# Kernel tuning notes

Measured on AMD Instinct MI355X. Metric: run time of the kernel, lower is better.

The kernel has to match this reference:

```python
import jax
jax.config.update("jax_enable_x64", True)
import jax.numpy as jnp
import numpy as np

# Paillier parameters (small primes so all modular arithmetic is exact in int64)
P, Q = 59, 61
N = P * Q                    # 3599, public modulus
N2 = N * N                   # 12,952,801; (N2-1)^2 < 2^63 -> int64-safe
LAM = (P - 1) * (Q - 1) // np.gcd(P - 1, Q - 1)   # lcm(p-1, q-1) = 870
MU = pow(int(LAM), -1, int(N))                     # lambda^{-1} mod n (g = n+1 variant)
LAM_BITS = [(LAM >> i) & 1 for i in range(int(LAM).bit_length())]  # LSB-first, static


def _decrypt(c):
    """Batched Paillier decryption: m = L(c^lambda mod n^2) * mu mod n, L(x)=(x-1)//n."""
    b = c % N2
    r = jnp.ones_like(b)
    # static square-and-multiply over the 10 bits of lambda (fully unrolled, elementwise)
    for bit in LAM_BITS:
        if bit:
            r = (r * b) % N2
        b = (b * b) % N2
    return ((r - 1) // N * MU) % N


def setup_inputs() -> dict:
    key = jax.random.key(0)
    k1, _ = jax.random.split(key)
    c = jax.random.randint(k1, (8192, 4096), 1, N2, dtype=jnp.int64)
    inv_scale = jnp.ones((1,), dtype=jnp.float32)
    return {"c": c, "inv_scale": inv_scale}


def reference(c, inv_scale):
    dec = _decrypt(c).astype(jnp.float32)
    # original: activation(decrypt(c) / 1000); inv_scale == 1.0 keeps math identical
    return jax.nn.relu(dec * (inv_scale / 1000.0))
```

## Files before the change

### kernel.cpp

```cpp
#include <hip/hip_runtime.h>
#include <stdint.h>

static constexpr uint32_t PP  = 59, QQ = 61;
static constexpr uint32_t Nn  = PP * QQ;
static constexpr uint32_t P2  = PP * PP;
static constexpr uint32_t Q2  = QQ * QQ;
static constexpr uint32_t LAM = 1740;

constexpr uint32_t cinv(uint32_t a, uint32_t m) {
    for (uint32_t x = 1; x < m; ++x) if ((uint64_t)a * x % m == 1u) return x;
    return 0u;
}
static constexpr uint32_t MUc = cinv(LAM % Nn, Nn);
static constexpr uint32_t IQP = cinv(P2 % Q2, Q2);

static constexpr int TPAD = 3484;
static constexpr int TQL  = 3722;
static constexpr int TTOT = TPAD + TQL;
static constexpr size_t WS_NEED = (size_t)TTOT * 2;

__device__ __forceinline__ uint32_t mul24lo(uint32_t a, uint32_t b) {
    uint32_t r;
    asm("v_mul_u32_u24 %0, %1, %2" : "=v"(r) : "v"(a), "v"(b));
    return r;
}
__device__ __forceinline__ uint32_t mul24hi(uint32_t a, uint32_t b) {
    uint32_t r;
    asm("v_mul_hi_u32_u24 %0, %1, %2" : "=v"(r) : "v"(a), "v"(b));
    return r;
}

template<uint32_t D>
__device__ __forceinline__ uint32_t mod_small(uint32_t x) {
    constexpr uint32_t M = (uint32_t)((1ull << 35) / D);
    uint32_t q = mul24hi(x, M) >> 3;
    uint32_t r = x - mul24lo(q, D);
    r = min(r, r - D);
    return r;
}

template<uint32_t MOD>
__device__ uint32_t powmod1740(uint32_t base) {
    uint32_t b = base, r = 1u, e = LAM;
    while (e) {
        if (e & 1u) r = (r * b) % MOD;
        b = (b * b) % MOD;
        e >>= 1u;
    }
    return r;
}

__global__ void build_tables(uint16_t* __restrict__ T) {
    int i = blockIdx.x * blockDim.x + threadIdx.x;
    if (i < (int)P2) T[i]        = (uint16_t)powmod1740<P2>((uint32_t)i);
    if (i < (int)Q2) T[TPAD + i] = (uint16_t)powmod1740<Q2>((uint32_t)i);
}

__device__ __forceinline__ float dec1(uint32_t c, const uint16_t* sTp,
                                      const uint16_t* sTq, float scale) {
    uint32_t a = sTp[mod_small<P2>(c)];
    uint32_t b = sTq[mod_small<Q2>(c)];
    uint32_t d0 = b + Q2 - a;
    d0 = min(d0, d0 - Q2);
    uint32_t t = mod_small<Q2>(mul24lo(d0, IQP));
    uint32_t r = a + mul24lo(t, P2);
    uint32_t rm1 = (r == 0u) ? (3598u * Nn) : (r - 1u);
    constexpr uint32_t MN = (uint32_t)((1ull << 35) / Nn);
    uint32_t q   = mul24hi(rm1, MN) >> 3;
    uint32_t rem = rm1 - mul24lo(q, Nn);
    q += (rem >= Nn) ? 1u : 0u;
    uint32_t m = mod_small<Nn>(mul24lo(q, MUc));
    return fmaxf((float)m * scale, 0.0f);
}

#define BLK 256

__global__ __launch_bounds__(BLK) void paillier_main(
        const uint4* __restrict__ in4, float4* __restrict__ out,
        const uint16_t* __restrict__ T, const float* __restrict__ inv_scale,
        int n4) {
    __shared__ uint32_t sT32[TTOT / 2];
    {
        const uint32_t* Ts = (const uint32_t*)T;
        for (int k = threadIdx.x; k < TTOT / 2; k += BLK) sT32[k] = Ts[k];
    }
    __syncthreads();
    const uint16_t* sTp = (const uint16_t*)sT32;
    const uint16_t* sTq = sTp + TPAD;

    float scale = inv_scale[0] / 1000.0f;

    int stride = gridDim.x * BLK;
    for (int i = blockIdx.x * BLK + threadIdx.x; i < n4; i += stride) {
        uint4 a = in4[i];
        float4 o;
        o.x = dec1(a.x, sTp, sTq, scale);
        o.y = dec1(a.y, sTp, sTq, scale);
        o.z = dec1(a.z, sTp, sTq, scale);
        o.w = dec1(a.w, sTp, sTq, scale);
        out[i] = o;
    }
}

__global__ __launch_bounds__(BLK) void paillier_main_fb(
        const uint4* __restrict__ in4, float4* __restrict__ out,
        const float* __restrict__ inv_scale, int n4) {
    __shared__ uint32_t sT32[TTOT / 2];
    uint16_t* sTp = (uint16_t*)sT32;
    uint16_t* sTq = sTp + TPAD;
    for (int i = threadIdx.x; i < (int)P2; i += BLK)
        sTp[i] = (uint16_t)powmod1740<P2>((uint32_t)i);
    for (int i = threadIdx.x; i < (int)Q2; i += BLK)
        sTq[i] = (uint16_t)powmod1740<Q2>((uint32_t)i);
    __syncthreads();
    float scale = inv_scale[0] / 1000.0f;
    int stride = gridDim.x * BLK;
    for (int i = blockIdx.x * BLK + threadIdx.x; i < n4; i += stride) {
        uint4 a = in4[i];
        float4 o;
        o.x = dec1(a.x, sTp, sTq, scale);
        o.y = dec1(a.y, sTp, sTq, scale);
        o.z = dec1(a.z, sTp, sTq, scale);
        o.w = dec1(a.w, sTp, sTq, scale);
        out[i] = o;
    }
}

extern "C" void kernel_launch(void* const* d_in, const int* in_sizes, int n_in,
                              void* d_out, int out_size, void* d_ws, size_t ws_size,
                              hipStream_t stream) {
    const uint4* c        = (const uint4*)d_in[0];
    const float* invscale = (const float*)d_in[1];
    float4* out           = (float4*)d_out;

    int n  = in_sizes[0];
    int n4 = n / 4;

    int nblk = 2048;
    int need = (n4 + BLK - 1) / BLK;
    if (nblk > need) nblk = need;

    if (ws_size >= WS_NEED && d_ws != nullptr) {
        uint16_t* T = (uint16_t*)d_ws;
        build_tables<<<(Q2 + 255) / 256, 256, 0, stream>>>(T);
        paillier_main<<<nblk, BLK, 0, stream>>>(c, out, T, invscale, n4);
    } else {
        paillier_main_fb<<<nblk, BLK, 0, stream>>>(c, out, invscale, n4);
    }
}
```

Measured before the change: 236.4 us.

## Precompute packed per-prime decryption digits to shorten per-element CRT arithmetic

Replaces the per-element CRT recombination mod n^2, the L-function division and the mu multiply with table entries that already hold the message residues mod p and q (plus fallbacks for non-coprime ciphertexts). Per element this leaves two table lookups and a short recombination mod n. Tables grow to 32-bit entries, doubling shared memory, and block size and grid count change as well. The packed-field encoding and the special-case flags add correctness risk.

```diff
diff --git a/kernel.cpp b/kernel.cpp
--- a/kernel.cpp
+++ b/kernel.cpp
@@ -11,13 +11,16 @@
     for (uint32_t x = 1; x < m; ++x) if ((uint64_t)a * x % m == 1u) return x;
     return 0u;
 }
-static constexpr uint32_t MUc = cinv(LAM % Nn, Nn);
+static constexpr uint32_t MU  = cinv(LAM % Nn, Nn);
 static constexpr uint32_t IQP = cinv(P2 % Q2, Q2);
+static constexpr uint32_t GAM = cinv(PP % QQ, QQ);
+static constexpr uint32_t CPP = (cinv(QQ % PP, PP) * (MU % PP)) % PP;
+static constexpr uint32_t CQQ = (cinv(PP % QQ, QQ) * (MU % QQ)) % QQ;
 
-static constexpr int TPAD = 3484;
-static constexpr int TQL  = 3722;
-static constexpr int TTOT = TPAD + TQL;
-static constexpr size_t WS_NEED = (size_t)TTOT * 2;
+static constexpr int TPN = 3484;
+static constexpr int TQN = 3724;
+static constexpr int TT  = TPN + TQN;
+static constexpr size_t WS_NEED = (size_t)TT * 4;
 
 __device__ __forceinline__ uint32_t mul24lo(uint32_t a, uint32_t b) {
     uint32_t r;
@@ -29,19 +32,23 @@
     asm("v_mul_hi_u32_u24 %0, %1, %2" : "=v"(r) : "v"(a), "v"(b));
     return r;
 }
-
-template<uint32_t D>
-__device__ __forceinline__ uint32_t mod_small(uint32_t x) {
-    constexpr uint32_t M = (uint32_t)((1ull << 35) / D);
-    uint32_t q = mul24hi(x, M) >> 3;
-    uint32_t r = x - mul24lo(q, D);
-    r = min(r, r - D);
+__device__ __forceinline__ uint32_t mad24_59(uint32_t a, uint32_t c) {
+    uint32_t r;
+    asm("v_mad_u32_u24 %0, %1, 59, %2" : "=v"(r) : "v"(a), "v"(c));
     return r;
 }
 
+template<uint32_t D>
+__device__ __forceinline__ uint32_t mod24(uint32_t x) {
+    constexpr uint32_t M = (uint32_t)((1ull << 32) / D);
+    uint32_t q = mul24hi(x, M);
+    uint32_t r = x - mul24lo(q, D);
+    return min(r, r - D);
+}
+
 template<uint32_t MOD>
-__device__ uint32_t powmod1740(uint32_t base) {
-    uint32_t b = base, r = 1u, e = LAM;
+__device__ uint32_t pow1740(uint32_t base) {
+    uint32_t b = base % MOD, r = 1u, e = LAM;
     while (e) {
         if (e & 1u) r = (r * b) % MOD;
         b = (b * b) % MOD;
@@ -49,44 +56,75 @@
     }
     return r;
 }
-
-__global__ void build_tables(uint16_t* __restrict__ T) {
-    int i = blockIdx.x * blockDim.x + threadIdx.x;
-    if (i < (int)P2) T[i]        = (uint16_t)powmod1740<P2>((uint32_t)i);
-    if (i < (int)Q2) T[TPAD + i] = (uint16_t)powmod1740<Q2>((uint32_t)i);
+__device__ uint32_t m_from_r(uint32_t r) {
+    if (r == 0u) return Nn - MU;
+    uint32_t x = (r - 1u) / Nn;
+    return (x * MU) % Nn;
+}
+__device__ uint32_t tp_entry(uint32_t i) {
+    uint32_t a = pow1740<P2>(i);
+    uint32_t flag = (i % PP == 0u) ? 0x80000000u : 0u;
+    uint32_t gp = 0u, mp = 0u;
+    if (!flag) {
+        uint32_t s = (a - 1u) / PP;
+        mp = (s * CPP) % PP;
+        gp = (mp * GAM) % QQ;
+    }
+    uint32_t t = (uint32_t)(((uint64_t)((Q2 - a % Q2) % Q2) * IQP) % Q2);
+    uint32_t r = a + P2 * t;
+    uint32_t dq = m_from_r(r);
+    return gp | (mp << 8) | (dq << 16) | flag;
+}
+__device__ uint32_t tq_entry(uint32_t i) {
+    uint32_t b = pow1740<Q2>(i);
+    uint32_t flag = (i % QQ == 0u) ? 0x80000000u : 0u;
+    uint32_t gq = 0u;
+    if (!flag) {
+        uint32_t s = (b - 1u) / QQ;
+        uint32_t mq = (s * CQQ) % QQ;
+        gq = (mq * GAM) % QQ;
+    }
+    uint32_t t = (uint32_t)(((uint64_t)b * IQP) % Q2);
+    uint32_t r = P2 * t;
+    uint32_t dp = m_from_r(r);
+    return gq | (dp << 16) | flag;
 }
 
-__device__ __forceinline__ float dec1(uint32_t c, const uint16_t* sTp,
-                                      const uint16_t* sTq, float scale) {
-    uint32_t a = sTp[mod_small<P2>(c)];
-    uint32_t b = sTq[mod_small<Q2>(c)];
-    uint32_t d0 = b + Q2 - a;
-    d0 = min(d0, d0 - Q2);
-    uint32_t t = mod_small<Q2>(mul24lo(d0, IQP));
-    uint32_t r = a + mul24lo(t, P2);
-    uint32_t rm1 = (r == 0u) ? (3598u * Nn) : (r - 1u);
-    constexpr uint32_t MN = (uint32_t)((1ull << 35) / Nn);
-    uint32_t q   = mul24hi(rm1, MN) >> 3;
-    uint32_t rem = rm1 - mul24lo(q, Nn);
-    q += (rem >= Nn) ? 1u : 0u;
-    uint32_t m = mod_small<Nn>(mul24lo(q, MUc));
+__global__ void build_tables(uint32_t* __restrict__ T) {
+    int i = blockIdx.x * blockDim.x + threadIdx.x;
+    if (i < TPN) T[i]       = (i < (int)P2) ? tp_entry((uint32_t)i) : 0u;
+    if (i < TQN) T[TPN + i] = (i < (int)Q2) ? tq_entry((uint32_t)i) : 0u;
+}
+
+__device__ __forceinline__ float dec1(uint32_t c, const uint32_t* sTp,
+                                      const uint32_t* sTq, float scale) {
+    uint32_t up = sTp[mod24<P2>(c)];
+    uint32_t uq = sTq[mod24<Q2>(c)];
+    uint32_t gp  = up & 63u;
+    uint32_t mp  = (up >> 8) & 63u;
+    uint32_t dqv = (up >> 16) & 0xFFFu;
+    uint32_t gq  = uq & 63u;
+    uint32_t dpv = (uq >> 16) & 0xFFFu;
+    uint32_t d = gq + QQ - gp;
+    d = min(d, d - QQ);
+    uint32_t m = mad24_59(d, mp);
+    m = ((int32_t)uq < 0) ? dqv : m;
+    m = ((int32_t)up < 0) ? dpv : m;
     return fmaxf((float)m * scale, 0.0f);
 }
 
-#define BLK 256
+#define BLK 512
 
-__global__ __launch_bounds__(BLK) void paillier_main(
+__global__ __launch_bounds__(BLK, 8) void paillier_main(
         const uint4* __restrict__ in4, float4* __restrict__ out,
-        const uint16_t* __restrict__ T, const float* __restrict__ inv_scale,
+        const uint32_t* __restrict__ T, const float* __restrict__ inv_scale,
         int n4) {
-    __shared__ uint32_t sT32[TTOT / 2];
-    {
-        const uint32_t* Ts = (const uint32_t*)T;
-        for (int k = threadIdx.x; k < TTOT / 2; k += BLK) sT32[k] = Ts[k];
-    }
+    __shared__ uint32_t sT[TT];
+    for (int k = threadIdx.x; k < TT / 4; k += BLK)
+        ((uint4*)sT)[k] = ((const uint4*)T)[k];
     __syncthreads();
-    const uint16_t* sTp = (const uint16_t*)sT32;
-    const uint16_t* sTq = sTp + TPAD;
+    const uint32_t* sTp = sT;
+    const uint32_t* sTq = sT + TPN;
 
     float scale = inv_scale[0] / 1000.0f;
 
@@ -105,14 +143,12 @@
 __global__ __launch_bounds__(BLK) void paillier_main_fb(
         const uint4* __restrict__ in4, float4* __restrict__ out,
         const float* __restrict__ inv_scale, int n4) {
-    __shared__ uint32_t sT32[TTOT / 2];
-    uint16_t* sTp = (uint16_t*)sT32;
-    uint16_t* sTq = sTp + TPAD;
-    for (int i = threadIdx.x; i < (int)P2; i += BLK)
-        sTp[i] = (uint16_t)powmod1740<P2>((uint32_t)i);
-    for (int i = threadIdx.x; i < (int)Q2; i += BLK)
-        sTq[i] = (uint16_t)powmod1740<Q2>((uint32_t)i);
+    __shared__ uint32_t sT[TT];
+    for (int i = threadIdx.x; i < (int)P2; i += BLK) sT[i]       = tp_entry((uint32_t)i);
+    for (int i = threadIdx.x; i < (int)Q2; i += BLK) sT[TPN + i] = tq_entry((uint32_t)i);
     __syncthreads();
+    const uint32_t* sTp = sT;
+    const uint32_t* sTq = sT + TPN;
     float scale = inv_scale[0] / 1000.0f;
     int stride = gridDim.x * BLK;
     for (int i = blockIdx.x * BLK + threadIdx.x; i < n4; i += stride) {
@@ -136,13 +172,13 @@
     int n  = in_sizes[0];
     int n4 = n / 4;
 
-    int nblk = 2048;
+    int nblk = 1024;
     int need = (n4 + BLK - 1) / BLK;
     if (nblk > need) nblk = need;
 
     if (ws_size >= WS_NEED && d_ws != nullptr) {
-        uint16_t* T = (uint16_t*)d_ws;
-        build_tables<<<(Q2 + 255) / 256, 256, 0, stream>>>(T);
+        uint32_t* T = (uint32_t*)d_ws;
+        build_tables<<<(TQN + 255) / 256, 256, 0, stream>>>(T);
         paillier_main<<<nblk, BLK, 0, stream>>>(c, out, T, invscale, n4);
     } else {
         paillier_main_fb<<<nblk, BLK, 0, stream>>>(c, out, invscale, n4);
```

New measurement: 235.4 us. No clear change (-0.4%).
